# Optimization experiments

Measured on AMD Instinct MI355X. Metric: run time of the kernel, lower is better.

Reference implementation:

```python
import jax, jax.numpy as jnp
import numpy as np

EPS_BN = 1e-5

def _grid_sample(fea, gx, gy):
    # fea: [B,C,H,W]; gx,gy: [B,P] normalized to [-1,1]; bilinear, zeros padding, align_corners=True
    B, C, H, W = fea.shape
    x = (gx + 1.0) * 0.5 * (W - 1)
    y = (gy + 1.0) * 0.5 * (H - 1)
    x0 = jnp.floor(x)
    y0 = jnp.floor(y)
    wx1 = x - x0
    wy1 = y - y0
    flat = fea.reshape(B, C, H * W)
    def tap(xi, yi, w):
        valid = ((xi >= 0) & (xi <= W - 1) & (yi >= 0) & (yi <= H - 1)).astype(fea.dtype)
        xi_c = jnp.clip(xi, 0, W - 1).astype(jnp.int32)
        yi_c = jnp.clip(yi, 0, H - 1).astype(jnp.int32)
        g = jnp.take_along_axis(flat, (yi_c * W + xi_c)[:, None, :], axis=2)  # [B,C,P]
        return g * (w * valid)[:, None, :]
    return (tap(x0, y0, (1 - wx1) * (1 - wy1)) + tap(x0 + 1, y0, wx1 * (1 - wy1))
            + tap(x0, y0 + 1, (1 - wx1) * wy1) + tap(x0 + 1, y0 + 1, wx1 * wy1))

def _homo_warp(src_fea, src_proj, ref_proj, depth_values):
    # src_fea: [B,C,H,W] -> warped [B,C,D,H,W] (MVSNet homo_warping, grid under stop_gradient)
    B, C, H, W = src_fea.shape
    D = depth_values.shape[1]
    proj = jnp.matmul(src_proj, jnp.linalg.inv(ref_proj))
    rot, trans = proj[:, :3, :3], proj[:, :3, 3]
    yy, xx = jnp.meshgrid(jnp.arange(H, dtype=src_fea.dtype), jnp.arange(W, dtype=src_fea.dtype), indexing='ij')
    xyz = jnp.stack([xx.ravel(), yy.ravel(), jnp.ones(H * W, src_fea.dtype)], 0)  # [3,HW]
    rot_xyz = jnp.einsum('bij,jp->bip', rot, xyz)  # [B,3,HW]
    pxyz = rot_xyz[:, :, None, :] * depth_values.reshape(B, 1, D, H * W) + trans[:, :, None, None]  # [B,3,D,HW]
    z = pxyz[:, 2]
    gx = jax.lax.stop_gradient(((pxyz[:, 0] / z) / ((W - 1) / 2.0) - 1.0).reshape(B, D * H * W))
    gy = jax.lax.stop_gradient(((pxyz[:, 1] / z) / ((H - 1) / 2.0) - 1.0).reshape(B, D * H * W))
    return _grid_sample(src_fea, gx, gy).reshape(B, C, D, H, W)

def _pixelwise_net(x, w0, g0, b0, m0, v0, w1, g1, b1, m1, v1, w2, b2):
    # x: [B,1,D,H,W]; 1x1x1 Conv3d(bias=False)+BN+ReLU twice, then Conv3d(8->1)+sigmoid+max over D
    def bnrelu(h, g, b, m, v):
        s = (1, -1, 1, 1, 1)
        return jax.nn.relu((h - m.reshape(s)) * (g / jnp.sqrt(v + EPS_BN)).reshape(s) + b.reshape(s))
    h = bnrelu(jnp.einsum('oc,bcdhw->bodhw', w0, x), g0, b0, m0, v0)
    h = bnrelu(jnp.einsum('oc,bcdhw->bodhw', w1, h), g1, b1, m1, v1)
    h = jnp.einsum('oc,bcdhw->bodhw', w2, h) + b2.reshape(1, -1, 1, 1, 1)
    out = jax.nn.sigmoid(h[:, 0])  # [B,D,H,W]
    return jnp.max(out, axis=1, keepdims=True)  # [B,1,H,W]

def _forward(features, proj_matrices, depth_values, num_depth,
             pw_w0, pw_g0, pw_b0, pw_m0, pw_v0, pw_w1, pw_g1, pw_b1, pw_m1, pw_v1, pw_w2, pw_b2,
             reg_w, reg_b):
    ref_fea = features[0]
    B, C, H, W = ref_fea.shape
    V = features.shape[0]
    D = num_depth
    def proj_new(p):  # p: [B,2,4,4] -> K @ E on top 3 rows
        top = jnp.matmul(p[:, 1, :3, :3], p[:, 0, :3, :4])
        return jnp.concatenate([top, p[:, 0, 3:4, :]], axis=1)
    ref_proj_new = proj_new(proj_matrices[:, 0])
    sim_sum = jnp.zeros((B, 1, D, H, W), ref_fea.dtype)
    w_sum = jnp.full((B, 1, 1, H, W), 1e-5, ref_fea.dtype)
    vw_list = []
    for i in range(1, V):  # small fixed loop over source views
        src_proj_new = proj_new(proj_matrices[:, i])
        warped = _homo_warp(features[i], src_proj_new, ref_proj_new, depth_values)
        sim = jnp.mean(warped * ref_fea[:, :, None], axis=1, keepdims=True)  # [B,1,D,H,W]
        vw = _pixelwise_net(sim, pw_w0, pw_g0, pw_b0, pw_m0, pw_v0, pw_w1, pw_g1, pw_b1, pw_m1, pw_v1, pw_w2, pw_b2)
        vw_list.append(vw)
        sim_sum = sim_sum + sim * vw[:, :, None]
        w_sum = w_sum + vw[:, :, None]
    similarity = sim_sum / w_sum
    cost_reg = jax.lax.conv_general_dilated(similarity, reg_w, (1, 1, 1), 'SAME',
                                            dimension_numbers=('NCDHW', 'OIDHW', 'NCDHW')) + reg_b.reshape(1, -1, 1, 1, 1)
    prob_volume = jax.nn.softmax(cost_reg[:, 0], axis=1)  # exp(log_softmax) == softmax
    idx = jnp.argmax(prob_volume, axis=1, keepdims=True)
    depth = jnp.take_along_axis(depth_values, idx, axis=1)[:, 0]  # WTA depth [B,H,W]
    conf = jnp.max(prob_volume, axis=1)
    view_weights = jnp.concatenate(vw_list, axis=1)
    return depth, conf, prob_volume, cost_reg, view_weights

def setup_inputs():
    key = jax.random.key(0)
    ks = jax.random.split(key, 20)
    B, V, C, H, W, D = 2, 5, 32, 128, 160, 32
    features = jax.random.normal(ks[0], (V, B, C, H, W), jnp.float32)
    K = np.eye(4, dtype=np.float32)
    K[0, 0] = 180.0; K[1, 1] = 180.0; K[0, 2] = W / 2.0; K[1, 2] = H / 2.0
    pm = np.zeros((B, V, 2, 4, 4), np.float32)
    for v in range(V):
        E = np.eye(4, dtype=np.float32)
        E[0, 3] = 10.0 * v  # horizontal baseline per source view
        pm[:, v, 0] = E
        pm[:, v, 1] = K
    depth_values = jnp.broadcast_to(jnp.linspace(425.0, 935.0, D, dtype=jnp.float32)[None, :, None, None], (B, D, H, W)) + 0.0
    rn = lambda k, s, sc=0.3: jax.random.normal(k, s, jnp.float32) * sc
    return {
        'features': features,
        'proj_matrices': jnp.asarray(pm),
        'depth_values': depth_values,
        'num_depth': D,
        'pw_w0': rn(ks[1], (16, 1)),
        'pw_g0': 1.0 + rn(ks[2], (16,), 0.1), 'pw_b0': rn(ks[3], (16,), 0.1),
        'pw_m0': rn(ks[4], (16,), 0.1), 'pw_v0': 1.0 + 0.5 * jax.random.uniform(ks[5], (16,)),
        'pw_w1': rn(ks[6], (8, 16)),
        'pw_g1': 1.0 + rn(ks[7], (8,), 0.1), 'pw_b1': rn(ks[8], (8,), 0.1),
        'pw_m1': rn(ks[9], (8,), 0.1), 'pw_v1': 1.0 + 0.5 * jax.random.uniform(ks[10], (8,)),
        'pw_w2': rn(ks[11], (1, 8)),
        'pw_b2': rn(ks[12], (1,), 0.1),
        'reg_w': rn(ks[13], (1, 1, 3, 3, 3), 0.1),
        'reg_b': rn(ks[14], (1,), 0.1),
    }

def reference(features, proj_matrices, depth_values, num_depth,
              pw_w0, pw_g0, pw_b0, pw_m0, pw_v0, pw_w1, pw_g1, pw_b1, pw_m1, pw_v1, pw_w2, pw_b2,
              reg_w, reg_b):
    return _forward(features, proj_matrices, depth_values, num_depth,
                    pw_w0, pw_g0, pw_b0, pw_m0, pw_v0, pw_w1, pw_g1, pw_b1, pw_m1, pw_v1, pw_w2, pw_b2,
                    reg_w, reg_b)
```

## Files before the change

kernel.cpp:

```cpp
#include <hip/hip_runtime.h>
#include <math.h>

#define BB 2
#define VV 5
#define CC 32
#define HH 128
#define WW 160
#define DD 32
#define HWp (HH*WW)
#define NV (VV-1)
#define PX 16
#define MAXSLOT 18

#define OFF_RT   0
#define OFF_PRM  96
#define OFF_FEAT 512
#define OFF_SIM  (OFF_FEAT + VV*BB*HWp*CC)
#define OFF_T    (OFF_SIM + BB*DD*HWp)
#define OFF_TAB  (OFF_T + 16)
#define OFF_FLAG (OFF_TAB + 17*16)

#define OUT_DEPTH 0
#define OUT_CONF  (BB*HWp)
#define OUT_PROB  (2*BB*HWp)
#define OUT_COST  (OUT_PROB + BB*DD*HWp)
#define OUT_VW    (OUT_COST + BB*DD*HWp)

__device__ void build_proj(const float* proj, int b, int v, double M[4][4]) {
    const float* E = proj + (((b*VV + v)*2 + 0)*16);
    const float* K = proj + (((b*VV + v)*2 + 1)*16);
    for (int r = 0; r < 3; r++)
        for (int c = 0; c < 4; c++) {
            double s = 0.0;
            for (int k = 0; k < 3; k++) s += (double)K[r*4+k] * (double)E[k*4+c];
            M[r][c] = s;
        }
    for (int c = 0; c < 4; c++) M[3][c] = (double)E[12+c];
}

__device__ void inv4(const double M[4][4], double out[4][4]) {
    double a[4][8];
    for (int i = 0; i < 4; i++)
        for (int j = 0; j < 4; j++) { a[i][j] = M[i][j]; a[i][4+j] = (i == j) ? 1.0 : 0.0; }
    for (int col = 0; col < 4; col++) {
        int piv = col; double best = fabs(a[col][col]);
        for (int r = col+1; r < 4; r++) if (fabs(a[r][col]) > best) { best = fabs(a[r][col]); piv = r; }
        if (piv != col) for (int j = 0; j < 8; j++) { double t = a[col][j]; a[col][j] = a[piv][j]; a[piv][j] = t; }
        double dinv = 1.0 / a[col][col];
        for (int j = 0; j < 8; j++) a[col][j] *= dinv;
        for (int r = 0; r < 4; r++) {
            if (r == col) continue;
            double f = a[r][col];
            for (int j = 0; j < 8; j++) a[r][j] -= f * a[col][j];
        }
    }
    for (int i = 0; i < 4; i++) for (int j = 0; j < 4; j++) out[i][j] = a[i][4+j];
}

__global__ __launch_bounds__(256) void setup_kernel(const float* __restrict__ proj,
    const float* __restrict__ w0, const float* __restrict__ g0, const float* __restrict__ b0,
    const float* __restrict__ m0, const float* __restrict__ v0,
    const float* __restrict__ w1, const float* __restrict__ g1, const float* __restrict__ b1,
    const float* __restrict__ m1, const float* __restrict__ v1,
    const float* __restrict__ w2, const float* __restrict__ b2,
    float* __restrict__ ws) {
    __shared__ float prmL[177];
    __shared__ float TL[16];
    int t = threadIdx.x;

    if (t < BB*NV) {
        int b = t / NV, v = 1 + (t % NV);
        double refM[4][4], inv[4][4], S[4][4];
        build_proj(proj, b, 0, refM);
        inv4(refM, inv);
        build_proj(proj, b, v, S);
        float* rt = ws + OFF_RT + (b*NV + (v-1))*12;
        for (int r = 0; r < 3; r++) {
            for (int c = 0; c < 3; c++) {
                double s = 0.0;
                for (int k = 0; k < 4; k++) s += S[r][k] * inv[k][c];
                rt[r*3 + c] = (float)s;
            }
            double s = 0.0;
            for (int k = 0; k < 4; k++) s += S[r][k] * inv[k][3];
            rt[9 + r] = (float)s;
        }
    }

    if (t < 16) {
        float sc = g0[t] / sqrtf(v0[t] + 1e-5f);
        prmL[t]      = w0[t] * sc;
        prmL[16 + t] = b0[t] - m0[t] * sc;
    }
    if (t >= 32 && t < 160) {
        int i = t - 32, q = i >> 4, o = i & 15;
        float sc = g1[q] / sqrtf(v1[q] + 1e-5f);
        prmL[32 + q*16 + o] = w1[q*16 + o] * sc;
    }
    if (t >= 160 && t < 168) {
        int q = t - 160;
        float sc = g1[q] / sqrtf(v1[q] + 1e-5f);
        prmL[160 + q] = b1[q] - m1[q] * sc;
        prmL[168 + q] = w2[q];
    }
    if (t == 176) prmL[176] = b2[0];
    __syncthreads();

    if (t < BB) {
        int ok = 1;
        for (int i = 0; i < NV; i++) {
            const float* ri = ws + OFF_RT + (t*NV + i)*12;
            ok &= (fabsf(ri[6])        < 1e-6f);
            ok &= (fabsf(ri[7])        < 1e-6f);
            ok &= (fabsf(ri[8] - 1.f)  < 1e-6f);
            ok &= (fabsf(ri[10])       < 1e-6f);
            ok &= (fabsf(ri[11])       < 1e-6f);
        }
        ws[OFF_FLAG + t] = ok ? 1.f : 0.f;
    }

    if (t == 0) {
        float tmp[16]; int nk = 0;
        for (int o = 0; o < 16; o++) {
            float a = prmL[o];
            if (a != 0.f) tmp[nk++] = -prmL[16+o] / a;
        }
        for (int i = 1; i < nk; i++) {
            float key = tmp[i]; int j = i-1;
            while (j >= 0 && tmp[j] > key) { tmp[j+1] = tmp[j]; j--; }
            tmp[j+1] = key;
        }
        for (int i = 0; i < 16; i++) TL[i] = (i < nk) ? tmp[i] : 3.4e38f;
    }
    __syncthreads();

    if (t < 17*8) {
        int seg = t >> 3, q = t & 7;
        float lo = (seg == 0)  ? -1e30f : TL[seg-1];
        float hi = (seg == 16) ?  1e30f : TL[seg];
        float smid;
        if (hi > 1e29f)       smid = lo + 1.f;
        else if (lo < -1e29f) smid = hi - 1.f;
        else                  smid = 0.5f*(lo + hi);
        float alpha = 0.f, beta = prmL[160+q];
        #pragma unroll
        for (int o = 0; o < 16; o++) {
            float a = prmL[o], c = prmL[16+o];
            if (a*smid + c > 0.f) {
                alpha += prmL[32+q*16+o]*a;
                beta  += prmL[32+q*16+o]*c;
            }
        }
        ws[OFF_TAB + seg*16 + q]     = alpha;
        ws[OFF_TAB + seg*16 + 8 + q] = beta;
    }
    if (t < 177) ws[OFF_PRM + t] = prmL[t];
    if (t < 16)  ws[OFF_T + t]   = TL[t];
}

__global__ __launch_bounds__(256) void transpose_kernel(const float* __restrict__ fea,
                                                        float* __restrict__ featT) {
    int t = blockIdx.x*256 + threadIdx.x;
    int w = t % WW;
    int h = (t / WW) % HH;
    int b = (t / (WW*HH)) % BB;
    int v = t / (WW*HH*BB);
    const float* src = fea + (size_t)((v*BB + b)*CC) * HWp + h*WW + w;
    float* dst = featT + (size_t)((v*BB + b)*HWp + h*WW + w) * CC;
    #pragma unroll
    for (int c = 0; c < CC; c += 4) {
        float4 q;
        q.x = src[(c+0)*HWp];
        q.y = src[(c+1)*HWp];
        q.z = src[(c+2)*HWp];
        q.w = src[(c+3)*HWp];
        *reinterpret_cast<float4*>(dst + c) = q;
    }
}

__device__ __forceinline__ float half_max(float v) {
    v = fmaxf(v, __shfl_xor(v, 1));
    v = fmaxf(v, __shfl_xor(v, 2));
    v = fmaxf(v, __shfl_xor(v, 4));
    v = fmaxf(v, __shfl_xor(v, 8));
    v = fmaxf(v, __shfl_xor(v, 16));
    return v;
}

__device__ __forceinline__ float dot32(const float* __restrict__ col,
                                       const float* __restrict__ refp) {
    float acc = 0.f;
    #pragma unroll
    for (int c = 0; c < CC; c += 4) {
        float4 a = *reinterpret_cast<const float4*>(col + c);
        float4 r = *reinterpret_cast<const float4*>(refp + c);
        acc = fmaf(a.w, r.w, fmaf(a.z, r.z, fmaf(a.y, r.y, fmaf(a.x, r.x, acc))));
    }
    return acc;
}

__device__ __forceinline__ void mlp_out(
    float s0, float s1, float s2, float s3,
    int d2, int b, int p,
    const float* __restrict__ tabL, const float* __restrict__ Tg,
    const float* __restrict__ prm,
    float* __restrict__ out, float* __restrict__ simout) {
    float T0 = Tg[0], T1 = Tg[1], T2 = Tg[2], T3 = Tg[3];
    float T4 = Tg[4], T5 = Tg[5], T6 = Tg[6], T7 = Tg[7];
    float T8 = Tg[8], T9 = Tg[9], T10 = Tg[10], T11 = Tg[11];
    float T12 = Tg[12], T13 = Tg[13], T14 = Tg[14], T15 = Tg[15];
    float wq0 = prm[168], wq1 = prm[169], wq2 = prm[170], wq3 = prm[171];
    float wq4 = prm[172], wq5 = prm[173], wq6 = prm[174], wq7 = prm[175];
    float p176 = prm[176];

    float sv[NV] = {s0, s1, s2, s3};
    float vw[NV];
    #pragma unroll
    for (int v = 0; v < NV; v++) {
        float s = sv[v];
        int seg = 0;
        seg += (s > T0);  seg += (s > T1);  seg += (s > T2);  seg += (s > T3);
        seg += (s > T4);  seg += (s > T5);  seg += (s > T6);  seg += (s > T7);
        seg += (s > T8);  seg += (s > T9);  seg += (s > T10); seg += (s > T11);
        seg += (s > T12); seg += (s > T13); seg += (s > T14); seg += (s > T15);
        const float* row = &tabL[seg << 4];
        float4 A0 = *reinterpret_cast<const float4*>(row);
        float4 A1 = *reinterpret_cast<const float4*>(row + 4);
        float4 B0 = *reinterpret_cast<const float4*>(row + 8);
        float4 B1 = *reinterpret_cast<const float4*>(row + 12);
        float h2v = p176;
        h2v = fmaf(wq0, fmaxf(fmaf(A0.x, s, B0.x), 0.f), h2v);
        h2v = fmaf(wq1, fmaxf(fmaf(A0.y, s, B0.y), 0.f), h2v);
        h2v = fmaf(wq2, fmaxf(fmaf(A0.z, s, B0.z), 0.f), h2v);
        h2v = fmaf(wq3, fmaxf(fmaf(A0.w, s, B0.w), 0.f), h2v);
        h2v = fmaf(wq4, fmaxf(fmaf(A1.x, s, B1.x), 0.f), h2v);
        h2v = fmaf(wq5, fmaxf(fmaf(A1.y, s, B1.y), 0.f), h2v);
        h2v = fmaf(wq6, fmaxf(fmaf(A1.z, s, B1.z), 0.f), h2v);
        h2v = fmaf(wq7, fmaxf(fmaf(A1.w, s, B1.w), 0.f), h2v);
        float m = half_max(h2v);
        vw[v] = 1.f/(1.f + __expf(-m));
    }

    if (d2 == 0) out[OUT_VW + (b*NV + 0)*HWp + p] = vw[0];
    if (d2 == 1) out[OUT_VW + (b*NV + 1)*HWp + p] = vw[1];
    if (d2 == 2) out[OUT_VW + (b*NV + 2)*HWp + p] = vw[2];
    if (d2 == 3) out[OUT_VW + (b*NV + 3)*HWp + p] = vw[3];

    float wsum = 1e-5f + vw[0] + vw[1] + vw[2] + vw[3];
    float ssum = s0*vw[0] + s1*vw[1] + s2*vw[2] + s3*vw[3];
    simout[(b*DD + d2)*HWp + p] = ssum / wsum;
}

__device__ __forceinline__ float tap_blend(
    const float* __restrict__ vbv, int sub8, float sx,
    float ay0, float ay1, int r0, int r1,
    float4 rva, float4 rvb) {
    float x0f = floorf(sx);
    float wx1 = sx - x0f;
    float wx0 = 1.f - wx1;
    int xi0 = (int)x0f, xi1 = xi0 + 1;
    float ax0 = ((unsigned)xi0 < WW) ? wx0 : 0.f;
    float ax1 = ((unsigned)xi1 < WW) ? wx1 : 0.f;
    int xc0 = min(max(xi0, 0), WW-1);
    int xc1 = min(max(xi1, 0), WW-1);
    float w00 = ax0*ay0, w01 = ax1*ay0;
    const float* q00 = vbv + (((r0 + xc0) << 5) + sub8);
    const float* q01 = vbv + (((r0 + xc1) << 5) + sub8);
    float4 t00a = *reinterpret_cast<const float4*>(q00);
    float4 t00b = *reinterpret_cast<const float4*>(q00 + 4);
    float4 t01a = *reinterpret_cast<const float4*>(q01);
    float4 t01b = *reinterpret_cast<const float4*>(q01 + 4);

    float blx = fmaf(w01, t01a.x, w00*t00a.x);
    float bly = fmaf(w01, t01a.y, w00*t00a.y);
    float blz = fmaf(w01, t01a.z, w00*t00a.z);
    float blw = fmaf(w01, t01a.w, w00*t00a.w);
    float acc = fmaf(rva.w,blw, fmaf(rva.z,blz, fmaf(rva.y,bly, rva.x*blx)));
    blx = fmaf(w01, t01b.x, w00*t00b.x);
    bly = fmaf(w01, t01b.y, w00*t00b.y);
    blz = fmaf(w01, t01b.z, w00*t00b.z);
    blw = fmaf(w01, t01b.w, w00*t00b.w);
    acc = fmaf(rvb.w,blw, fmaf(rvb.z,blz, fmaf(rvb.y,bly, fmaf(rvb.x,blx, acc))));

    if (ay1 != 0.f) {
        float w10 = ax0*ay1, w11 = ax1*ay1;
        const float* q10 = vbv + (((r1 + xc0) << 5) + sub8);
        const float* q11 = vbv + (((r1 + xc1) << 5) + sub8);
        float4 t10a = *reinterpret_cast<const float4*>(q10);
        float4 t10b = *reinterpret_cast<const float4*>(q10 + 4);
        float4 t11a = *reinterpret_cast<const float4*>(q11);
        float4 t11b = *reinterpret_cast<const float4*>(q11 + 4);
        float cx = fmaf(w11, t11a.x, w10*t10a.x);
        float cy = fmaf(w11, t11a.y, w10*t10a.y);
        float cz = fmaf(w11, t11a.z, w10*t10a.z);
        float cw = fmaf(w11, t11a.w, w10*t10a.w);
        acc = fmaf(rva.w,cw, fmaf(rva.z,cz, fmaf(rva.y,cy, fmaf(rva.x,cx, acc))));
        cx = fmaf(w11, t11b.x, w10*t10b.x);
        cy = fmaf(w11, t11b.y, w10*t10b.y);
        cz = fmaf(w11, t11b.z, w10*t10b.z);
        cw = fmaf(w11, t11b.w, w10*t10b.w);
        acc = fmaf(rvb.w,cw, fmaf(rvb.z,cz, fmaf(rvb.y,cy, fmaf(rvb.x,cx, acc))));
    }
    return acc;
}

__global__ __launch_bounds__(256) void fused_sim_kernel(
    const float* __restrict__ featT, const float* __restrict__ rtAll,
    const float* __restrict__ prm, const float* __restrict__ Tg,
    const float* __restrict__ tabG, const float* __restrict__ flagG,
    const float* __restrict__ depthv,
    float* __restrict__ simout, float* __restrict__ out) {
    __shared__ float simL[NV][DD][PX+1];
    __shared__ float depthL[DD][PX+1];
    __shared__ float ziL[DD][PX+1];
    __shared__ float refLd[PX][36];
    __shared__ float gtabAll[NV][PX][MAXSLOT];
    __shared__ __align__(16) float tabL[17*16];
    __shared__ float ay0L[NV][PX], ay1L[NV][PX];
    __shared__ int   r0L[NV][PX], r1L[NV][PX], xbL[NV][PX], slotsL[NV][PX];
    __shared__ int   badF;

    int t = threadIdx.x;
    int b = blockIdx.y;
    int pbase = blockIdx.x * PX;
    int hi  = pbase / WW;
    int wi0 = pbase % WW;
    float fy = (float)hi;

    {
        int di = t >> 4, k = t & 15;
        float dep0 = depthv[(b*DD + di)*HWp + pbase + k];
        float dep1 = depthv[(b*DD + di + 16)*HWp + pbase + k];
        depthL[di][k] = dep0;      depthL[di+16][k] = dep1;
        ziL[di][k] = __builtin_amdgcn_rcpf(dep0);
        ziL[di+16][k] = __builtin_amdgcn_rcpf(dep1);
        refLd[di][k]      = featT[(size_t)(b*HWp + pbase + di)*CC + k];
        refLd[di][k+16]   = featT[(size_t)(b*HWp + pbase + di)*CC + k + 16];
        tabL[t] = tabG[t];
        if (t < 16) tabL[256 + t] = tabG[256 + t];
        if (t == 0) badF = 0;
    }
    __syncthreads();

    float rc[NV][12];
    #pragma unroll
    for (int v = 0; v < NV; v++)
        #pragma unroll
        for (int j = 0; j < 12; j++)
            rc[v][j] = rtAll[(b*NV + v)*12 + j];
    float bx0[NV], by0[NV], bz0[NV];
    #pragma unroll
    for (int v = 0; v < NV; v++) {
        bx0[v] = fmaf((float)wi0, rc[v][0], fmaf(fy, rc[v][1], rc[v][2]));
        by0[v] = fmaf((float)wi0, rc[v][3], fmaf(fy, rc[v][4], rc[v][5]));
        bz0[v] = fmaf((float)wi0, rc[v][6], fmaf(fy, rc[v][7], rc[v][8]));
    }
    bool fast = (flagG[b] != 0.f);

    if (fast) {
        int p_loc = t >> 5;
        int d = t & 31;
        for (int ph = 0; ph < 2; ph++) {
            int p = ph*8 + p_loc;
            float fk = (float)p;
            float zi = ziL[d][p];
            #pragma unroll
            for (int v = 0; v < NV; v++) {
                float bx = fmaf(fk, rc[v][0], bx0[v]);
                float sx = fmaf(rc[v][9], zi, bx);
                float mn = sx, mx = sx;
                #pragma unroll
                for (int off = 1; off <= 16; off <<= 1) {
                    mn = fminf(mn, __shfl_xor(mn, off));
                    mx = fmaxf(mx, __shfl_xor(mx, off));
                }
                if (d == 0) {
                    float by = fmaf(fk, rc[v][3], by0[v]);
                    float sy = by;
                    float sny = rintf(sy);
                    sy = (fabsf(sy - sny) < 1e-4f) ? sny : sy;
                    float y0f = floorf(sy);
                    float wy1 = sy - y0f, wy0 = 1.f - wy1;
                    int yi0 = (int)y0f, yi1 = yi0 + 1;
                    ay0L[v][p] = ((unsigned)yi0 < HH) ? wy0 : 0.f;
                    ay1L[v][p] = ((unsigned)yi1 < HH) ? wy1 : 0.f;
                    r0L[v][p] = min(max(yi0, 0), HH-1)*WW;
                    r1L[v][p] = min(max(yi1, 0), HH-1)*WW;
                    bool finite = (mn > -1e9f) && (mx < 1e9f) && (mn == mn) && (mx == mx);
                    int xb = finite ? (int)floorf(mn) : 0;
                    int slots = finite ? ((int)floorf(mx) - xb + 2) : MAXSLOT + 1;
                    xbL[v][p] = xb;
                    slotsL[v][p] = slots;
                    if (slots > MAXSLOT) badF = 1;
                }
            }
        }
        __syncthreads();
        fast = (badF == 0);
    }

    if (fast) {
        {
            int v2 = t & 3, p2 = (t >> 2) & 15, i0 = t >> 6;
            float ay0 = ay0L[v2][p2], ay1 = ay1L[v2][p2];
            int r0 = r0L[v2][p2], r1 = r1L[v2][p2];
            int xb = xbL[v2][p2], slots = slotsL[v2][p2];
            const float* vbv = featT + (size_t)(((v2+1)*BB + b)*HWp)*CC;
            const float* refp = &refLd[p2][0];
            for (int i2 = i0; i2 < slots; i2 += 4) {
                int xc = min(max(xb + i2, 0), WW-1);
                float g = ay0 * dot32(vbv + ((r0 + xc) << 5), refp);
                if (ay1 != 0.f) g = fmaf(ay1, dot32(vbv + ((r1 + xc) << 5), refp), g);
                gtabAll[v2][p2][i2] = g * (1.f/(float)CC);
            }
        }
        __syncthreads();
        {
            int p_loc = t >> 5, d = t & 31;
            for (int ph = 0; ph < 2; ph++) {
                int p = ph*8 + p_loc;
                float fk = (float)p;
                float zi = ziL[d][p];
                float sv[NV];
                #pragma unroll
                for (int v = 0; v < NV; v++) {
                    float bx = fmaf(fk, rc[v][0], bx0[v]);
                    float sx = fmaf(rc[v][9], zi, bx);
                    float x0f = floorf(sx);
                    float wx1 = sx - x0f, wx0 = 1.f - wx1;
                    int xi0 = (int)x0f, xi1 = xi0 + 1;
                    float ax0 = ((unsigned)xi0 < WW) ? wx0 : 0.f;
                    float ax1 = ((unsigned)xi1 < WW) ? wx1 : 0.f;
                    int ii = xi0 - xbL[v][p];
                    float g0 = gtabAll[v][p][ii];
                    float g1 = gtabAll[v][p][ii+1];
                    sv[v] = fmaf(ax0, g0, ax1*g1);
                }
                mlp_out(sv[0], sv[1], sv[2], sv[3], d, b, pbase + p,
                        tabL, Tg, prm, out, simout);
            }
        }
        return;
    }

    {
        int sub = t & 3;
        int dB  = (t >> 2) & 31;
        int kk  = t >> 7;
        int sub8 = sub*8;
        #pragma unroll 2
        for (int j = 0; j < PX/2; j++) {
            int kpix = j*2 + kk;
            int p = pbase + kpix;
            float fk = (float)kpix;
            float depth = depthL[dB][kpix];
            const float* refp = featT + (size_t)(b*HWp + p)*CC + sub8;
            float4 rva = *reinterpret_cast<const float4*>(refp);
            float4 rvb = *reinterpret_cast<const float4*>(refp + 4);

            #pragma unroll
            for (int v = 0; v < NV; v++) {
                float bx = fmaf(fk, rc[v][0], bx0[v]);
                float by = fmaf(fk, rc[v][3], by0[v]);
                float bz = fmaf(fk, rc[v][6], bz0[v]);
                float px = fmaf(bx, depth, rc[v][9]);
                float py = fmaf(by, depth, rc[v][10]);
                float pz = fmaf(bz, depth, rc[v][11]);
                float zi = __builtin_amdgcn_rcpf(pz);
                float sx = px * zi, sy = py * zi;
                float sny = rintf(sy);
                sy = (fabsf(sy - sny) < 1e-4f) ? sny : sy;
                float y0f = floorf(sy);
                float wy1 = sy - y0f, wy0 = 1.f - wy1;
                int yi0 = (int)y0f, yi1 = yi0 + 1;
                float ay0 = ((unsigned)yi0 < HH) ? wy0 : 0.f;
                float ay1 = ((unsigned)yi1 < HH) ? wy1 : 0.f;
                int yc0 = min(max(yi0, 0), HH-1);
                int yc1 = min(max(yi1, 0), HH-1);
                int r0 = yc0*WW, r1 = yc1*WW;
                const float* vbv = featT + (size_t)(((v+1)*BB + b)*HWp)*CC;
                float acc = tap_blend(vbv, sub8, sx, ay0, ay1, r0, r1, rva, rvb);
                acc += __shfl_xor(acc, 1);
                acc += __shfl_xor(acc, 2);
                if (sub == 0) simL[v][dB][kpix] = acc * (1.f/(float)CC);
            }
        }
        __syncthreads();

        int p8 = t >> 5;
        int d2 = t & 31;
        #pragma unroll
        for (int pi = 0; pi < PX/8; pi++) {
            int pidx = pi*8 + p8;
            mlp_out(simL[0][d2][pidx], simL[1][d2][pidx],
                    simL[2][d2][pidx], simL[3][d2][pidx],
                    d2, b, pbase + pidx, tabL, Tg, prm, out, simout);
        }
    }
}

__global__ __launch_bounds__(256) void convsm_kernel(
    const float* __restrict__ sim, const float* __restrict__ rw,
    const float* __restrict__ rb, const float* __restrict__ depthv,
    float* __restrict__ out) {
    __shared__ float tile[34*121 + 7];
    int t = threadIdx.x;
    int tw = blockIdx.x * 8;
    int th = blockIdx.y * 8;
    int b  = blockIdx.z;

    for (int i = t; i < 34*120; i += 256) {
        int e = i / 120; int rem = i % 120;
        int h = rem / 12, w = rem % 12;
        int gd = e - 1, gh = th + h - 1, gw = tw + w - 1;
        float v = 0.f;
        if (w < 10 && gd >= 0 && gd < DD && (unsigned)gh < HH && (unsigned)gw < WW)
            v = sim[((b*DD + gd)*HH + gh)*WW + gw];
        tile[e*121 + rem] = v;
    }
    __syncthreads();

    float wk[27];
    #pragma unroll
    for (int i = 0; i < 27; i++) wk[i] = rw[i];
    float bias = rb[0];

    int p  = t >> 2, dq = t & 3;
    int ph = p >> 3, pw = p & 7;
    int d0 = dq * 8;

    float cost[8];
    #pragma unroll
    for (int j = 0; j < 8; j++) cost[j] = bias;
    #pragma unroll
    for (int e = 0; e < 10; e++) {
        int el = d0 + e;
        float s0 = 0.f, s1 = 0.f, s2 = 0.f;
        #pragma unroll
        for (int kh = 0; kh < 3; kh++) {
            #pragma unroll
            for (int kw = 0; kw < 3; kw++) {
                float x = tile[el*121 + (ph+kh)*12 + (pw+kw)];
                s0 = fmaf(wk[0*9 + kh*3 + kw], x, s0);
                s1 = fmaf(wk[1*9 + kh*3 + kw], x, s1);
                s2 = fmaf(wk[2*9 + kh*3 + kw], x, s2);
            }
        }
        if (e < 8)            cost[e]   += s0;
        if (e >= 1 && e <= 8) cost[e-1] += s1;
        if (e >= 2)           cost[e-2] += s2;
    }

    int pg = (th + ph)*WW + (tw + pw);
    #pragma unroll
    for (int j = 0; j < 8; j++)
        out[OUT_COST + (b*DD + d0 + j)*HWp + pg] = cost[j];

    float m = cost[0]; int mi = d0;
    #pragma unroll
    for (int j = 1; j < 8; j++) { if (cost[j] > m) { m = cost[j]; mi = d0 + j; } }
    #pragma unroll
    for (int off = 1; off <= 2; off <<= 1) {
        float m2 = __shfl_xor(m, off);
        int  i2 = __shfl_xor(mi, off);
        if (m2 > m || (m2 == m && i2 < mi)) { m = m2; mi = i2; }
    }
    float sum = 0.f;
    float e8[8];
    #pragma unroll
    for (int j = 0; j < 8; j++) { e8[j] = __expf(cost[j] - m); sum += e8[j]; }
    #pragma unroll
    for (int off = 1; off <= 2; off <<= 1) sum += __shfl_xor(sum, off);
    float inv = 1.f / sum;
    #pragma unroll
    for (int j = 0; j < 8; j++)
        out[OUT_PROB + (b*DD + d0 + j)*HWp + pg] = e8[j] * inv;
    if (dq == 0) {
        out[OUT_DEPTH + b*HWp + pg] = depthv[(b*DD + mi)*HWp + pg];
        out[OUT_CONF  + b*HWp + pg] = inv;
    }
}

extern "C" void kernel_launch(void* const* d_in, const int* in_sizes, int n_in,
                              void* d_out, int out_size, void* d_ws, size_t ws_size,
                              hipStream_t stream) {
    const float* features = (const float*)d_in[0];
    const float* proj     = (const float*)d_in[1];
    const float* depthv   = (const float*)d_in[2];
    const float* w0 = (const float*)d_in[4];
    const float* g0 = (const float*)d_in[5];
    const float* b0 = (const float*)d_in[6];
    const float* m0 = (const float*)d_in[7];
    const float* v0 = (const float*)d_in[8];
    const float* w1 = (const float*)d_in[9];
    const float* g1 = (const float*)d_in[10];
    const float* b1 = (const float*)d_in[11];
    const float* m1 = (const float*)d_in[12];
    const float* v1 = (const float*)d_in[13];
    const float* w2 = (const float*)d_in[14];
    const float* b2 = (const float*)d_in[15];
    const float* rw = (const float*)d_in[16];
    const float* rb = (const float*)d_in[17];
    float* out = (float*)d_out;
    float* ws  = (float*)d_ws;

    setup_kernel<<<1, 256, 0, stream>>>(proj, w0, g0, b0, m0, v0, w1, g1, b1, m1, v1, w2, b2, ws);
    transpose_kernel<<<VV*BB*HWp/256, 256, 0, stream>>>(features, ws + OFF_FEAT);

    fused_sim_kernel<<<dim3(HWp/PX, BB), 256, 0, stream>>>(
        ws + OFF_FEAT, ws + OFF_RT, ws + OFF_PRM, ws + OFF_T, ws + OFF_TAB,
        ws + OFF_FLAG, depthv, ws + OFF_SIM, out);

    convsm_kernel<<<dim3(WW/8, HH/8, BB), 256, 0, stream>>>(
        ws + OFF_SIM, rw, rb, depthv, out);
}
```

Baseline: 88.86 us.

## Merge setup into transpose kernel and union fused kernel shared memory

Folds the single-block setup kernel into block 0 of the transpose kernel, removing one launch. In the fused similarity kernel, the separate shared arrays for the fast and fallback paths are overlaid in one union buffer, which cuts LDS use per block so more blocks can be resident. The fallback path reloads depth into the shared buffer when the fast path bails out. The risk is that block 0 of the transpose now carries the serial setup work, and the overlaid buffers depend on correct restaging.

```diff
diff --git a/kernel.cpp b/kernel.cpp
--- a/kernel.cpp
+++ b/kernel.cpp
@@ -25,6 +25,19 @@
 #define OUT_PROB  (2*BB*HWp)
 #define OUT_COST  (OUT_PROB + BB*DD*HWp)
 #define OUT_VW    (OUT_COST + BB*DD*HWp)
+
+#define ZI(d,k)     smemU[(d)*17 + (k)]
+#define DEP(d,k)    smemU[(d)*17 + (k)]
+#define REF(p,c)    smemU[544 + (p)*36 + (c)]
+#define GT(v,p,i)   smemU[1120 + ((v)*16 + (p))*18 + (i)]
+#define AY0(v,p)    smemU[2272 + (v)*16 + (p)]
+#define AY1(v,p)    smemU[2336 + (v)*16 + (p)]
+#define IR0(v,p)    smemI[2400 + (v)*16 + (p)]
+#define IR1(v,p)    smemI[2464 + (v)*16 + (p)]
+#define IXB(v,p)    smemI[2528 + (v)*16 + (p)]
+#define ISL(v,p)    smemI[2592 + (v)*16 + (p)]
+#define BADF        smemI[2656]
+#define SIMG(v,d,p) smemU[544 + (((v)*32 + (d))*17 + (p))]
 
 __device__ void build_proj(const float* proj, int b, int v, double M[4][4]) {
     const float* E = proj + (((b*VV + v)*2 + 0)*16);
@@ -57,16 +70,14 @@
     for (int i = 0; i < 4; i++) for (int j = 0; j < 4; j++) out[i][j] = a[i][4+j];
 }
 
-__global__ __launch_bounds__(256) void setup_kernel(const float* __restrict__ proj,
+__device__ void setup_body(const float* __restrict__ proj,
     const float* __restrict__ w0, const float* __restrict__ g0, const float* __restrict__ b0,
     const float* __restrict__ m0, const float* __restrict__ v0,
     const float* __restrict__ w1, const float* __restrict__ g1, const float* __restrict__ b1,
     const float* __restrict__ m1, const float* __restrict__ v1,
     const float* __restrict__ w2, const float* __restrict__ b2,
-    float* __restrict__ ws) {
-    __shared__ float prmL[177];
-    __shared__ float TL[16];
-    int t = threadIdx.x;
+    float* __restrict__ ws, int t,
+    float* __restrict__ prmL, float* __restrict__ TL) {
 
     if (t < BB*NV) {
         int b = t / NV, v = 1 + (t % NV);
@@ -158,8 +169,21 @@
     if (t < 16)  ws[OFF_T + t]   = TL[t];
 }
 
-__global__ __launch_bounds__(256) void transpose_kernel(const float* __restrict__ fea,
-                                                        float* __restrict__ featT) {
+__global__ __launch_bounds__(256) void transpose_setup_kernel(
+    const float* __restrict__ fea, float* __restrict__ featT,
+    const float* __restrict__ proj,
+    const float* __restrict__ w0, const float* __restrict__ g0, const float* __restrict__ b0,
+    const float* __restrict__ m0, const float* __restrict__ v0,
+    const float* __restrict__ w1, const float* __restrict__ g1, const float* __restrict__ b1,
+    const float* __restrict__ m1, const float* __restrict__ v1,
+    const float* __restrict__ w2, const float* __restrict__ b2,
+    float* __restrict__ ws) {
+    __shared__ float prmL[177];
+    __shared__ float TL[16];
+    if (blockIdx.x == 0)
+        setup_body(proj, w0, g0, b0, m0, v0, w1, g1, b1, m1, v1, w2, b2,
+                   ws, threadIdx.x, prmL, TL);
+
     int t = blockIdx.x*256 + threadIdx.x;
     int w = t % WW;
     int h = (t / WW) % HH;
@@ -310,15 +334,9 @@
     const float* __restrict__ tabG, const float* __restrict__ flagG,
     const float* __restrict__ depthv,
     float* __restrict__ simout, float* __restrict__ out) {
-    __shared__ float simL[NV][DD][PX+1];
-    __shared__ float depthL[DD][PX+1];
-    __shared__ float ziL[DD][PX+1];
-    __shared__ float refLd[PX][36];
-    __shared__ float gtabAll[NV][PX][MAXSLOT];
+    __shared__ __align__(16) float smemU[2720];
     __shared__ __align__(16) float tabL[17*16];
-    __shared__ float ay0L[NV][PX], ay1L[NV][PX];
-    __shared__ int   r0L[NV][PX], r1L[NV][PX], xbL[NV][PX], slotsL[NV][PX];
-    __shared__ int   badF;
+    int* smemI = (int*)smemU;
 
     int t = threadIdx.x;
     int b = blockIdx.y;
@@ -327,18 +345,24 @@
     int wi0 = pbase % WW;
     float fy = (float)hi;
 
+    bool fast = (flagG[b] != 0.f);
+
     {
         int di = t >> 4, k = t & 15;
         float dep0 = depthv[(b*DD + di)*HWp + pbase + k];
         float dep1 = depthv[(b*DD + di + 16)*HWp + pbase + k];
-        depthL[di][k] = dep0;      depthL[di+16][k] = dep1;
-        ziL[di][k] = __builtin_amdgcn_rcpf(dep0);
-        ziL[di+16][k] = __builtin_amdgcn_rcpf(dep1);
-        refLd[di][k]      = featT[(size_t)(b*HWp + pbase + di)*CC + k];
-        refLd[di][k+16]   = featT[(size_t)(b*HWp + pbase + di)*CC + k + 16];
+        if (fast) {
+            ZI(di, k)    = __builtin_amdgcn_rcpf(dep0);
+            ZI(di+16, k) = __builtin_amdgcn_rcpf(dep1);
+            REF(di, k)      = featT[(size_t)(b*HWp + pbase + di)*CC + k];
+            REF(di, k+16)   = featT[(size_t)(b*HWp + pbase + di)*CC + k + 16];
+        } else {
+            DEP(di, k)    = dep0;
+            DEP(di+16, k) = dep1;
+        }
         tabL[t] = tabG[t];
         if (t < 16) tabL[256 + t] = tabG[256 + t];
-        if (t == 0) badF = 0;
+        if (t == 0 && fast) BADF = 0;
     }
     __syncthreads();
 
@@ -355,15 +379,14 @@
         by0[v] = fmaf((float)wi0, rc[v][3], fmaf(fy, rc[v][4], rc[v][5]));
         bz0[v] = fmaf((float)wi0, rc[v][6], fmaf(fy, rc[v][7], rc[v][8]));
     }
-    bool fast = (flagG[b] != 0.f);
-
+
+    bool needRestage = false;
     if (fast) {
-        int p_loc = t >> 5;
-        int d = t & 31;
+        int p_loc = t >> 5, d = t & 31;
         for (int ph = 0; ph < 2; ph++) {
             int p = ph*8 + p_loc;
             float fk = (float)p;
-            float zi = ziL[d][p];
+            float zi = ZI(d, p);
             #pragma unroll
             for (int v = 0; v < NV; v++) {
                 float bx = fmaf(fk, rc[v][0], bx0[v]);
@@ -382,36 +405,36 @@
                     float y0f = floorf(sy);
                     float wy1 = sy - y0f, wy0 = 1.f - wy1;
                     int yi0 = (int)y0f, yi1 = yi0 + 1;
-                    ay0L[v][p] = ((unsigned)yi0 < HH) ? wy0 : 0.f;
-                    ay1L[v][p] = ((unsigned)yi1 < HH) ? wy1 : 0.f;
-                    r0L[v][p] = min(max(yi0, 0), HH-1)*WW;
-                    r1L[v][p] = min(max(yi1, 0), HH-1)*WW;
+                    AY0(v, p) = ((unsigned)yi0 < HH) ? wy0 : 0.f;
+                    AY1(v, p) = ((unsigned)yi1 < HH) ? wy1 : 0.f;
+                    IR0(v, p) = min(max(yi0, 0), HH-1)*WW;
+                    IR1(v, p) = min(max(yi1, 0), HH-1)*WW;
                     bool finite = (mn > -1e9f) && (mx < 1e9f) && (mn == mn) && (mx == mx);
                     int xb = finite ? (int)floorf(mn) : 0;
                     int slots = finite ? ((int)floorf(mx) - xb + 2) : MAXSLOT + 1;
-                    xbL[v][p] = xb;
-                    slotsL[v][p] = slots;
-                    if (slots > MAXSLOT) badF = 1;
+                    IXB(v, p) = xb;
+                    ISL(v, p) = slots;
+                    if (slots > MAXSLOT) BADF = 1;
                 }
             }
         }
         __syncthreads();
-        fast = (badF == 0);
+        if (BADF) { fast = false; needRestage = true; }
     }
 
     if (fast) {
         {
             int v2 = t & 3, p2 = (t >> 2) & 15, i0 = t >> 6;
-            float ay0 = ay0L[v2][p2], ay1 = ay1L[v2][p2];
-            int r0 = r0L[v2][p2], r1 = r1L[v2][p2];
-            int xb = xbL[v2][p2], slots = slotsL[v2][p2];
+            float ay0 = AY0(v2, p2), ay1 = AY1(v2, p2);
+            int r0 = IR0(v2, p2), r1 = IR1(v2, p2);
+            int xb = IXB(v2, p2), slots = ISL(v2, p2);
             const float* vbv = featT + (size_t)(((v2+1)*BB + b)*HWp)*CC;
-            const float* refp = &refLd[p2][0];
+            const float* refp = &REF(p2, 0);
             for (int i2 = i0; i2 < slots; i2 += 4) {
                 int xc = min(max(xb + i2, 0), WW-1);
                 float g = ay0 * dot32(vbv + ((r0 + xc) << 5), refp);
                 if (ay1 != 0.f) g = fmaf(ay1, dot32(vbv + ((r1 + xc) << 5), refp), g);
-                gtabAll[v2][p2][i2] = g * (1.f/(float)CC);
+                GT(v2, p2, i2) = g * (1.f/(float)CC);
             }
         }
         __syncthreads();
@@ -420,7 +443,7 @@
             for (int ph = 0; ph < 2; ph++) {
                 int p = ph*8 + p_loc;
                 float fk = (float)p;
-                float zi = ziL[d][p];
+                float zi = ZI(d, p);
                 float sv[NV];
                 #pragma unroll
                 for (int v = 0; v < NV; v++) {
@@ -431,9 +454,9 @@
                     int xi0 = (int)x0f, xi1 = xi0 + 1;
                     float ax0 = ((unsigned)xi0 < WW) ? wx0 : 0.f;
                     float ax1 = ((unsigned)xi1 < WW) ? wx1 : 0.f;
-                    int ii = xi0 - xbL[v][p];
-                    float g0 = gtabAll[v][p][ii];
-                    float g1 = gtabAll[v][p][ii+1];
+                    int ii = xi0 - IXB(v, p);
+                    float g0 = GT(v, p, ii);
+                    float g1 = GT(v, p, ii+1);
                     sv[v] = fmaf(ax0, g0, ax1*g1);
                 }
                 mlp_out(sv[0], sv[1], sv[2], sv[3], d, b, pbase + p,
@@ -443,6 +466,12 @@
         return;
     }
 
+    if (needRestage) {
+        int di = t >> 4, k = t & 15;
+        DEP(di, k)    = depthv[(b*DD + di)*HWp + pbase + k];
+        DEP(di+16, k) = depthv[(b*DD + di + 16)*HWp + pbase + k];
+        __syncthreads();
+    }
     {
         int sub = t & 3;
         int dB  = (t >> 2) & 31;
@@ -453,7 +482,7 @@
             int kpix = j*2 + kk;
             int p = pbase + kpix;
             float fk = (float)kpix;
-            float depth = depthL[dB][kpix];
+            float depth = DEP(dB, kpix);
             const float* refp = featT + (size_t)(b*HWp + p)*CC + sub8;
             float4 rva = *reinterpret_cast<const float4*>(refp);
             float4 rvb = *reinterpret_cast<const float4*>(refp + 4);
@@ -482,7 +511,7 @@
                 float acc = tap_blend(vbv, sub8, sx, ay0, ay1, r0, r1, rva, rvb);
                 acc += __shfl_xor(acc, 1);
                 acc += __shfl_xor(acc, 2);
-                if (sub == 0) simL[v][dB][kpix] = acc * (1.f/(float)CC);
+                if (sub == 0) SIMG(v, dB, kpix) = acc * (1.f/(float)CC);
             }
         }
         __syncthreads();
@@ -492,8 +521,8 @@
         #pragma unroll
         for (int pi = 0; pi < PX/8; pi++) {
             int pidx = pi*8 + p8;
-            mlp_out(simL[0][d2][pidx], simL[1][d2][pidx],
-                    simL[2][d2][pidx], simL[3][d2][pidx],
+            mlp_out(SIMG(0, d2, pidx), SIMG(1, d2, pidx),
+                    SIMG(2, d2, pidx), SIMG(3, d2, pidx),
                     d2, b, pbase + pidx, tabL, Tg, prm, out, simout);
         }
     }
@@ -604,8 +633,9 @@
     float* out = (float*)d_out;
     float* ws  = (float*)d_ws;
 
-    setup_kernel<<<1, 256, 0, stream>>>(proj, w0, g0, b0, m0, v0, w1, g1, b1, m1, v1, w2, b2, ws);
-    transpose_kernel<<<VV*BB*HWp/256, 256, 0, stream>>>(features, ws + OFF_FEAT);
+    transpose_setup_kernel<<<VV*BB*HWp/256, 256, 0, stream>>>(
+        features, ws + OFF_FEAT, proj,
+        w0, g0, b0, m0, v0, w1, g1, b1, m1, v1, w2, b2, ws);
 
     fused_sim_kernel<<<dim3(HWp/PX, BB), 256, 0, stream>>>(
         ws + OFF_FEAT, ws + OFF_RT, ws + OFF_PRM, ws + OFF_T, ws + OFF_TAB,
```

Result: faster. 79.87 us (-10.1%).
